# Performance work log

Hardware: AMD Instinct MI355X
Metric: run time of the kernel (lower is better)

Reference implementation:

```python
import jax, jax.numpy as jnp
import numpy as np

T, B, I, H, NH = 256, 8, 1024, 1024, 16
DH = H // NH
LN_EPS = 1e-5


def setup_inputs() -> dict:
    key = jax.random.key(0)
    ks = jax.random.split(key, 8)
    def w(k, shape, fan_in):
        return jax.random.normal(k, shape, jnp.float32) / np.float32(np.sqrt(fan_in))
    inputs = jax.random.normal(ks[0], (T, B, I), jnp.float32)
    # 4 HybridGates (forget, input, update, output) stacked: Linear(I+H -> H)
    W_gates = w(ks[1], (4, H, I + H), I + H)
    b_gates = jnp.zeros((4, H), jnp.float32)
    ln_g = jnp.ones((4, H), jnp.float32)   # LayerNorm weight per gate
    ln_b = jnp.zeros((4, H), jnp.float32)  # LayerNorm bias per gate
    # MultiheadAttention in_proj (split into q/k/v) and out_proj
    Wq = w(ks[2], (H, H), H); Wk = w(ks[3], (H, H), H); Wv = w(ks[4], (H, H), H)
    bq = jnp.zeros((H,), jnp.float32); bk = jnp.zeros((H,), jnp.float32); bv = jnp.zeros((H,), jnp.float32)
    Wo = w(ks[5], (H, H), H); bo = jnp.zeros((H,), jnp.float32)
    return dict(inputs=inputs, W_gates=W_gates, b_gates=b_gates, ln_g=ln_g, ln_b=ln_b,
                Wq=Wq, Wk=Wk, Wv=Wv, bq=bq, bk=bk, bv=bv, Wo=Wo, bo=bo)


def _layernorm(x, g, b):
    m = jnp.mean(x, axis=-1, keepdims=True)
    v = jnp.var(x, axis=-1, keepdims=True)
    return (x - m) * jax.lax.rsqrt(v + LN_EPS) * g + b


def reference(inputs, W_gates, b_gates, ln_g, ln_b, Wq, Wk, Wv, bq, bk, bv, Wo, bo):
    Tn, Bn, _ = inputs.shape
    scale = 1.0 / np.float32(np.sqrt(DH))
    pos = jnp.arange(Tn)

    def step(carry, x_t):
        hx, cx, Kb, Vb, t = carry  # Kb/Vb: [T, B, NH, DH] cached projections of past outputs
        combined = jnp.concatenate([x_t, hx], axis=1)          # [B, I+H]
        z = jnp.einsum('bd,khd->kbh', combined, W_gates) + b_gates[:, None, :]
        z = _layernorm(z, ln_g[:, None, :], ln_b[:, None, :])  # [4, B, H]
        f = jax.nn.sigmoid(z[0]); i = jax.nn.sigmoid(z[1])
        g = jnp.tanh(z[2]);       o = jax.nn.sigmoid(z[3])
        cx = f * cx + i * g
        h0 = o * jnp.tanh(cx)                                   # [B, H]
        # attention of current hidden over all previously produced outputs
        q = (h0 @ Wq.T + bq).reshape(Bn, NH, DH)
        scores = jnp.einsum('bhd,sbhd->bhs', q, Kb) * scale     # [B, NH, T]
        scores = jnp.where((pos < t)[None, None, :], scores, -1e9)
        attn = jax.nn.softmax(scores, axis=-1)
        ctx = jnp.einsum('bhs,sbhd->bhd', attn, Vb).reshape(Bn, H)
        attn_out = ctx @ Wo.T + bo
        hx = h0 + jnp.where(t > 0, attn_out, 0.0)               # no attention at t=0
        # cache k/v projections of the new output (linear, so per-token projection is exact)
        Kb = Kb.at[t].set((hx @ Wk.T + bk).reshape(Bn, NH, DH))
        Vb = Vb.at[t].set((hx @ Wv.T + bv).reshape(Bn, NH, DH))
        return (hx, cx, Kb, Vb, t + 1), hx

    init = (jnp.zeros((Bn, H), inputs.dtype), jnp.zeros((Bn, H), inputs.dtype),
            jnp.zeros((Tn, Bn, NH, DH), inputs.dtype), jnp.zeros((Tn, Bn, NH, DH), inputs.dtype),
            jnp.int32(0))
    (hx, cx, _, _, _), outputs = jax.lax.scan(step, init, inputs)
    return outputs, hx, cx
```

## Files before the change

kernel.cpp:

```cpp
#include <hip/hip_runtime.h>
#include <math.h>

#define NBLK 256
#define NTHR 512
#define GATHER 255

#define OFF_HX    0
#define OFF_H0    8192
#define OFF_CTX   16384
#define OFF_Z     24576
#define OFF_KB    57344
#define OFF_VB    (OFF_KB + 2097152)
#define OFF_FLAGS (OFF_VB + 2097152)
#define FLG_U32   (4096 + 128 + 2048)

#define S_WG    0
#define S_STAGE 32768
#define S_CX    36864
#define S_H0L   37888
#define S_Q     38912
#define S_PS    38976
#define S_RED   39232
#define S_R2    39248
#define S_EH    39264
#define S_ZX    39296
#define S_KVX   39424
#define LDS_FLOATS 39488
#define LDS_BYTES  (LDS_FLOATS * 4)

typedef unsigned long long u64;
union F2U { u64 u; float2 f; };

__device__ __forceinline__ float ld1(const float* p) {
    return __hip_atomic_load(const_cast<float*>(p), __ATOMIC_RELAXED, __HIP_MEMORY_SCOPE_AGENT);
}
__device__ __forceinline__ void st1(float* p, float v) {
    __hip_atomic_store(p, v, __ATOMIC_RELAXED, __HIP_MEMORY_SCOPE_AGENT);
}
__device__ __forceinline__ unsigned ldu(const unsigned* p) {
    return __hip_atomic_load(const_cast<unsigned*>(p), __ATOMIC_RELAXED, __HIP_MEMORY_SCOPE_AGENT);
}
__device__ __forceinline__ void stu(unsigned* p, unsigned v) {
    __hip_atomic_store(p, v, __ATOMIC_RELAXED, __HIP_MEMORY_SCOPE_AGENT);
}
__device__ __forceinline__ float2 ld2(const float* p) {
    F2U c; c.u = __hip_atomic_load(reinterpret_cast<u64*>(const_cast<float*>(p)),
                                   __ATOMIC_RELAXED, __HIP_MEMORY_SCOPE_AGENT);
    return c.f;
}
__device__ __forceinline__ void st2(float* p, float2 v) {
    F2U c; c.f = v;
    __hip_atomic_store(reinterpret_cast<u64*>(p), c.u,
                       __ATOMIC_RELAXED, __HIP_MEMORY_SCOPE_AGENT);
}
__device__ __forceinline__ float4 ld4(const float* p) {
    float2 a = ld2(p), b = ld2(p + 2);
    return make_float4(a.x, a.y, b.x, b.y);
}
__device__ __forceinline__ float dot4(const float4 a, const float4 b) {
    return a.x*b.x + a.y*b.y + a.z*b.z + a.w*b.w;
}

__device__ __forceinline__ void arrive(unsigned* flags, int blk, unsigned bc) {
    __syncthreads();
    if (threadIdx.x == 0) stu(flags + blk * 16, bc);
}
__device__ __forceinline__ void waitbar(unsigned* flags, unsigned* golines,
                                        unsigned bc, int blk) {
    if (blk == GATHER) {
        if (threadIdx.x < 256)
            while (ldu(flags + threadIdx.x * 16) < bc) __builtin_amdgcn_s_sleep(4);
        __syncthreads();
        if (threadIdx.x < 8) stu(golines + threadIdx.x * 16, bc);
    } else {
        if (threadIdx.x == 0)
            while (ldu(golines + (blk >> 5) * 16) < bc) __builtin_amdgcn_s_sleep(4);
    }
    __syncthreads();
}

__global__ __launch_bounds__(NTHR, 1)
void qlstm_kernel(const float* __restrict__ x,  const float* __restrict__ Wg,
                  const float* __restrict__ bg, const float* __restrict__ lng,
                  const float* __restrict__ lnb,const float* __restrict__ Wq,
                  const float* __restrict__ Wk, const float* __restrict__ Wv,
                  const float* __restrict__ bq, const float* __restrict__ bk,
                  const float* __restrict__ bv, const float* __restrict__ Wo,
                  const float* __restrict__ bo, float* __restrict__ out,
                  float* __restrict__ ws)
{
    extern __shared__ float lds[];
    const int blk = blockIdx.x, tid = threadIdx.x;
    const int w = tid >> 6, l = tid & 63;

    __builtin_amdgcn_fence(__ATOMIC_ACQUIRE, "agent");

    float* hx  = ws + OFF_HX;   float* h0g = ws + OFF_H0;
    float* ctx = ws + OFF_CTX;  float* z   = ws + OFF_Z;
    float* Kb  = ws + OFF_KB;   float* Vb  = ws + OFF_VB;
    unsigned* flags   = (unsigned*)(ws + OFF_FLAGS);
    unsigned* golines = flags + 4096;
    unsigned* cflg    = golines + 128;
    unsigned bc = 1;

    {
        const float* wsrc = Wg + (size_t)blk * 32768;
        #pragma unroll
        for (int j = 0; j < 16; ++j) {
            const int fi = j * 512 + tid;
            *(float4*)(lds + S_WG + fi * 4) = *(const float4*)(wsrc + fi * 4);
        }
    }
    const int kv_mat = blk >> 7;
    const int kv_h   = (blk & 127) * 8 + w;
    const float* kv_wrow = (kv_mat ? Wv : Wk) + (size_t)kv_h * 1024;
    float4 wkv[4];
    #pragma unroll
    for (int i = 0; i < 4; ++i) wkv[i] = *(const float4*)(kv_wrow + i * 256 + l * 4);
    const float kv_bias = (kv_mat ? bv : bk)[kv_h];
    const int g     = blk >> 6;
    const int hbase = (blk & 63) * 16;
    const int h0r   = hbase + 2 * w;
    const float bg0 = bg[g * 1024 + h0r], bg1 = bg[g * 1024 + h0r + 1];
    float lnw0[4], lnw1[4], lnb0v[4], lnb1v[4];
    #pragma unroll
    for (int g2 = 0; g2 < 4; ++g2) {
        lnw0[g2] = lng[g2 * 1024 + tid];       lnb0v[g2] = lnb[g2 * 1024 + tid];
        lnw1[g2] = lng[g2 * 1024 + 512 + tid]; lnb1v[g2] = lnb[g2 * 1024 + 512 + tid];
    }
    const int rg = blk >> 2, bp = blk & 3;
    const int er0 = rg * 16 + 2 * w;
    const int eb0 = bp * 2, eb1 = eb0 + 1;
    const float bor0 = bo[er0], bor1 = bo[er0 + 1];
    const int ab = blk >> 4, anh = blk & 15;
    const bool h0_writer = (blk < 128) && ((blk & 15) == 0);
    const int qdh = tid >> 3, qks = tid & 7;
    const float q_bias = (blk < 128) ? bq[anh * 64 + qdh] : 0.f;

    { const int gi = blk * NTHR + tid; if (gi < 8192) st1(hx + gi, 0.f); }
    if (tid < 256) *(float4*)(lds + S_CX + tid * 4) = make_float4(0,0,0,0);
    arrive(flags, blk, bc);

    for (int t = 0; t < 256; ++t) {
        float a0[8], a1[8];
        {
            const float* xt = x + (size_t)t * 8192;
            #pragma unroll
            for (int b = 0; b < 8; ++b) { a0[b] = 0.f; a1[b] = 0.f; }
            #pragma unroll
            for (int i = 0; i < 4; ++i) {
                const int k = i * 256 + l * 4;
                const float4 w0 = *(const float4*)(lds + S_WG + (2*w)   * 2048 + k);
                const float4 w1 = *(const float4*)(lds + S_WG + (2*w+1) * 2048 + k);
                #pragma unroll
                for (int b = 0; b < 8; ++b) {
                    const float4 a = *(const float4*)(xt + b * 1024 + k);
                    a0[b] += dot4(w0, a); a1[b] += dot4(w1, a);
                }
            }
        }
        waitbar(flags, golines, bc, blk);

        {
            float akv[8];
            #pragma unroll
            for (int b = 0; b < 8; ++b) akv[b] = 0.f;
            float2 hreg[8];
            #pragma unroll
            for (int c = 0; c < 2; ++c)
                #pragma unroll
                for (int j = 0; j < 4; ++j) {
                    const int idx = j * 512 + tid;
                    const int b = idx >> 8, off2 = idx & 255;
                    hreg[c * 4 + j] = ld2(hx + b * 1024 + c * 512 + off2 * 2);
                }
            #pragma unroll
            for (int c = 0; c < 2; ++c) {
                if (c) __syncthreads();
                #pragma unroll
                for (int j = 0; j < 4; ++j)
                    *(float2*)(lds + S_STAGE + (j * 512 + tid) * 2) = hreg[c * 4 + j];
                __syncthreads();
                #pragma unroll
                for (int ii = 0; ii < 2; ++ii) {
                    const int k = ii * 256 + l * 4;
                    const float4 w0 = *(const float4*)(lds + S_WG + (2*w)   * 2048 + 1024 + c * 512 + k);
                    const float4 w1 = *(const float4*)(lds + S_WG + (2*w+1) * 2048 + 1024 + c * 512 + k);
                    const float4 wk = wkv[c * 2 + ii];
                    #pragma unroll
                    for (int b = 0; b < 8; ++b) {
                        const float4 a = *(const float4*)(lds + S_STAGE + b * 512 + k);
                        a0[b] += dot4(w0, a); a1[b] += dot4(w1, a); akv[b] += dot4(wk, a);
                    }
                }
            }
            #pragma unroll
            for (int o = 1; o < 64; o <<= 1)
                #pragma unroll
                for (int b = 0; b < 8; ++b) {
                    a0[b]  += __shfl_xor(a0[b], o);
                    a1[b]  += __shfl_xor(a1[b], o);
                    akv[b] += __shfl_xor(akv[b], o);
                }
            if (l == 0) {
                #pragma unroll
                for (int b = 0; b < 8; ++b) {
                    lds[S_ZX + (2*w)   * 8 + b] = a0[b] + bg0;
                    lds[S_ZX + (2*w+1) * 8 + b] = a1[b] + bg1;
                    lds[S_KVX + w * 8 + b]      = akv[b] + kv_bias;
                }
            }
            __syncthreads();
            if (tid < 128) {
                const int h = tid & 15, b2 = tid >> 4;
                st1(z + (size_t)(g * 8 + b2) * 1024 + hbase + h, lds[S_ZX + h * 8 + b2]);
            } else if (tid < 192 && t > 0) {
                const int j = tid - 128;
                const int b2 = j >> 3, hh = j & 7;
                float* dst = kv_mat ? Vb : Kb;
                st1(dst + ((size_t)(t - 1) * 8 + b2) * 1024 + (blk & 127) * 8 + hh,
                    lds[S_KVX + hh * 8 + b2]);
            }
        }
        ++bc; arrive(flags, blk, bc);
        waitbar(flags, golines, bc, blk);

        if (blk < 128) {
            {
                float2 zreg[4];
                #pragma unroll
                for (int j = 0; j < 4; ++j) {
                    const int idx = j * 512 + tid;
                    const int g2 = idx >> 9, off2 = idx & 511;
                    zreg[j] = ld2(z + ((size_t)g2 * 8 + ab) * 1024 + off2 * 2);
                }
                #pragma unroll
                for (int j = 0; j < 4; ++j)
                    *(float2*)(lds + S_STAGE + (j * 512 + tid) * 2) = zreg[j];
            }
            __syncthreads();
            const int gt = w >> 1, hf = w & 1;
            float s = 0.f, q2s = 0.f;
            #pragma unroll
            for (int j = 0; j < 8; ++j) {
                const float v = lds[S_STAGE + gt * 1024 + hf * 512 + j * 64 + l];
                s += v; q2s += v * v;
            }
            #pragma unroll
            for (int o = 1; o < 64; o <<= 1) { s += __shfl_xor(s, o); q2s += __shfl_xor(q2s, o); }
            if (l == 0) { lds[S_RED + w] = s; lds[S_R2 + w] = q2s; }
            __syncthreads();
            float mean[4], rstd[4];
            #pragma unroll
            for (int g2 = 0; g2 < 4; ++g2) {
                const float ss = lds[S_RED + 2*g2] + lds[S_RED + 2*g2 + 1];
                const float qq = lds[S_R2  + 2*g2] + lds[S_R2  + 2*g2 + 1];
                const float m = ss * (1.f / 1024.f);
                mean[g2] = m;
                rstd[g2] = rsqrtf(qq * (1.f / 1024.f) - m * m + 1e-5f);
            }
            {
                float zv[4];
                #pragma unroll
                for (int g2 = 0; g2 < 4; ++g2)
                    zv[g2] = (lds[S_STAGE + g2 * 1024 + tid] - mean[g2]) * rstd[g2] * lnw0[g2] + lnb0v[g2];
                const float f  = 1.f / (1.f + __expf(-zv[0]));
                const float ii = 1.f / (1.f + __expf(-zv[1]));
                const float gg = tanhf(zv[2]);
                const float oo = 1.f / (1.f + __expf(-zv[3]));
                const float c  = f * lds[S_CX + tid] + ii * gg;
                lds[S_CX + tid] = c;
                const float ho = oo * tanhf(c);
                lds[S_H0L + tid] = ho;
                if (h0_writer) st1(h0g + ab * 1024 + tid, ho);
            }
            {
                float zv[4];
                #pragma unroll
                for (int g2 = 0; g2 < 4; ++g2)
                    zv[g2] = (lds[S_STAGE + g2 * 1024 + 512 + tid] - mean[g2]) * rstd[g2] * lnw1[g2] + lnb1v[g2];
                const float f  = 1.f / (1.f + __expf(-zv[0]));
                const float ii = 1.f / (1.f + __expf(-zv[1]));
                const float gg = tanhf(zv[2]);
                const float oo = 1.f / (1.f + __expf(-zv[3]));
                const float c  = f * lds[S_CX + 512 + tid] + ii * gg;
                lds[S_CX + 512 + tid] = c;
                const float ho = oo * tanhf(c);
                lds[S_H0L + 512 + tid] = ho;
                if (h0_writer) st1(h0g + ab * 1024 + 512 + tid, ho);
            }
            __syncthreads();
            {
                const float* wrow = Wq + (size_t)(anh * 64 + qdh) * 1024;
                float qa = 0.f;
                #pragma unroll 8
                for (int j = 0; j < 32; ++j) {
                    const int k = j * 32 + qks * 4;
                    qa += dot4(*(const float4*)(wrow + k), *(const float4*)(lds + S_H0L + k));
                }
                qa += __shfl_xor(qa, 1); qa += __shfl_xor(qa, 2); qa += __shfl_xor(qa, 4);
                if (qks == 0) lds[S_Q + qdh] = (qa + q_bias) * 0.125f;
            }
            __syncthreads();
            if (t > 0) {
                float sc = -1e30f;
                if (tid < t) {
                    const float* kr = Kb + ((size_t)tid * 8 + ab) * 1024 + anh * 64;
                    float d = 0.f;
                    #pragma unroll
                    for (int j = 0; j < 16; ++j) {
                        const float4 k4 = *(const float4*)(kr + j * 4);
                        d += k4.x*lds[S_Q + j*4]   + k4.y*lds[S_Q + j*4+1]
                           + k4.z*lds[S_Q + j*4+2] + k4.w*lds[S_Q + j*4+3];
                    }
                    sc = d;
                }
                float mx = sc;
                #pragma unroll
                for (int o = 1; o < 64; o <<= 1) mx = fmaxf(mx, __shfl_xor(mx, o));
                if (l == 0) lds[S_RED + w] = mx;
                __syncthreads();
                mx = lds[S_RED];
                #pragma unroll
                for (int j = 1; j < 8; ++j) mx = fmaxf(mx, lds[S_RED + j]);
                const float p = (tid < t) ? __expf(sc - mx) : 0.f;
                if (tid < 256) lds[S_PS + tid] = p;
                float ps = p;
                #pragma unroll
                for (int o = 1; o < 64; o <<= 1) ps += __shfl_xor(ps, o);
                if (l == 0) lds[S_R2 + w] = ps;
                __syncthreads();
                float tot = lds[S_R2];
                #pragma unroll
                for (int j = 1; j < 8; ++j) tot += lds[S_R2 + j];
                const float inv = 1.f / tot;
                const int dh2 = tid & 31, ss2 = tid >> 5;
                const float* vbase = Vb + (size_t)ab * 1024 + anh * 64 + dh2 * 2;
                float cax0 = 0.f, cay0 = 0.f, cax1 = 0.f, cay1 = 0.f;
                int s2 = ss2;
                for (; s2 + 48 < t; s2 += 64) {
                    const float2 va = *(const float2*)(vbase + (size_t)(s2)      * 8192);
                    const float2 vb = *(const float2*)(vbase + (size_t)(s2 + 16) * 8192);
                    const float2 vc = *(const float2*)(vbase + (size_t)(s2 + 32) * 8192);
                    const float2 vd = *(const float2*)(vbase + (size_t)(s2 + 48) * 8192);
                    const float pa = lds[S_PS + s2],      pb = lds[S_PS + s2 + 16];
                    const float pc = lds[S_PS + s2 + 32], pd = lds[S_PS + s2 + 48];
                    cax0 += pa * va.x; cay0 += pa * va.y;
                    cax1 += pb * vb.x; cay1 += pb * vb.y;
                    cax0 += pc * vc.x; cay0 += pc * vc.y;
                    cax1 += pd * vd.x; cay1 += pd * vd.y;
                }
                for (; s2 < t; s2 += 16) {
                    const float pp = lds[S_PS + s2];
                    const float2 v2 = *(const float2*)(vbase + (size_t)s2 * 8192);
                    cax0 += pp * v2.x; cay0 += pp * v2.y;
                }
                *(float2*)(lds + S_STAGE + tid * 2) = make_float2(cax0 + cax1, cay0 + cay1);
                __syncthreads();
                if (tid < 64) {
                    float v = 0.f;
                    #pragma unroll
                    for (int j = 0; j < 16; ++j) v += lds[S_STAGE + j * 64 + tid];
                    st1(ctx + ab * 1024 + anh * 64 + tid, v * inv);
                }
            }
            __syncthreads();
            if (tid == 0) stu(cflg + blk * 16, (unsigned)(t + 1));
        }

        {
            if (tid < 32) {
                const int pb = (tid < 16) ? eb0 : eb1;
                const unsigned* f = cflg + (pb * 16 + (tid & 15)) * 16;
                while (ldu(f) < (unsigned)(t + 1)) __builtin_amdgcn_s_sleep(2);
            }
            __syncthreads();
        }

        {
            if (tid < 16) {
                const int bsel = tid >> 3, hp = tid & 7;
                *(float2*)(lds + S_EH + bsel * 16 + hp * 2) =
                    ld2(h0g + (size_t)(eb0 + bsel) * 1024 + rg * 16 + hp * 2);
            }
            float o00 = 0.f, o01 = 0.f, o10 = 0.f, o11 = 0.f;
            if (t > 0) {
                float4 c0r[4], c1r[4];
                #pragma unroll
                for (int i = 0; i < 4; ++i) {
                    const int k = i * 256 + l * 4;
                    c0r[i] = ld4(ctx + (size_t)eb0 * 1024 + k);
                    c1r[i] = ld4(ctx + (size_t)eb1 * 1024 + k);
                }
                #pragma unroll
                for (int i = 0; i < 4; ++i) {
                    const int k = i * 256 + l * 4;
                    const float4 w0 = *(const float4*)(Wo + (size_t)er0 * 1024 + k);
                    const float4 w1 = *(const float4*)(Wo + (size_t)(er0+1) * 1024 + k);
                    o00 += dot4(w0, c0r[i]); o01 += dot4(w0, c1r[i]);
                    o10 += dot4(w1, c0r[i]); o11 += dot4(w1, c1r[i]);
                }
                #pragma unroll
                for (int o = 1; o < 64; o <<= 1) {
                    o00 += __shfl_xor(o00, o); o01 += __shfl_xor(o01, o);
                    o10 += __shfl_xor(o10, o); o11 += __shfl_xor(o11, o);
                }
            }
            __syncthreads();
            if (l == 0) {
                const float h00 = lds[S_EH + 2*w],      h10 = lds[S_EH + 2*w + 1];
                const float h01 = lds[S_EH + 16 + 2*w], h11 = lds[S_EH + 16 + 2*w + 1];
                const float v00 = (t > 0) ? h00 + o00 + bor0 : h00;
                const float v10 = (t > 0) ? h10 + o10 + bor1 : h10;
                const float v01 = (t > 0) ? h01 + o01 + bor0 : h01;
                const float v11 = (t > 0) ? h11 + o11 + bor1 : h11;
                st2(hx + eb0 * 1024 + er0, make_float2(v00, v10));
                st2(hx + eb1 * 1024 + er0, make_float2(v01, v11));
                *(float2*)(out + (size_t)t * 8192 + eb0 * 1024 + er0) = make_float2(v00, v10);
                *(float2*)(out + (size_t)t * 8192 + eb1 * 1024 + er0) = make_float2(v01, v11);
            }
        }
        ++bc; arrive(flags, blk, bc);
    }
    waitbar(flags, golines, bc, blk);

    if (h0_writer) {
        out[2097152 + 8192 + ab * 1024 + tid]       = lds[S_CX + tid];
        out[2097152 + 8192 + ab * 1024 + 512 + tid] = lds[S_CX + 512 + tid];
    }
    if (blk >= 136 && blk < 144) {
        const int b = blk - 136;
        out[2097152 + b * 1024 + tid]       = ld1(hx + b * 1024 + tid);
        out[2097152 + b * 1024 + 512 + tid] = ld1(hx + b * 1024 + 512 + tid);
    }
}

extern "C" void kernel_launch(void* const* d_in, const int* in_sizes, int n_in,
                              void* d_out, int out_size, void* d_ws, size_t ws_size,
                              hipStream_t stream) {
    const float* x   = (const float*)d_in[0];
    const float* Wg  = (const float*)d_in[1];
    const float* bg  = (const float*)d_in[2];
    const float* lng = (const float*)d_in[3];
    const float* lnb = (const float*)d_in[4];
    const float* Wq  = (const float*)d_in[5];
    const float* Wk  = (const float*)d_in[6];
    const float* Wv  = (const float*)d_in[7];
    const float* bq  = (const float*)d_in[8];
    const float* bk  = (const float*)d_in[9];
    const float* bv  = (const float*)d_in[10];
    const float* Wo  = (const float*)d_in[11];
    const float* bo  = (const float*)d_in[12];
    float* out = (float*)d_out;
    float* ws  = (float*)d_ws;

    static int attr_set = 0;
    if (!attr_set) {
        hipFuncSetAttribute((const void*)qlstm_kernel,
                            hipFuncAttributeMaxDynamicSharedMemorySize, LDS_BYTES);
        attr_set = 1;
    }
    hipMemsetAsync((char*)d_ws + (size_t)OFF_FLAGS * 4, 0, (size_t)FLG_U32 * 4, stream);

    void* args[] = { &x, &Wg, &bg, &lng, &lnb, &Wq, &Wk, &Wv,
                     &bq, &bk, &bv, &Wo, &bo, &out, &ws };
    hipLaunchCooperativeKernel((void*)qlstm_kernel, dim3(NBLK), dim3(NTHR),
                               args, LDS_BYTES, stream);
}
```

Measured before the change: 9.736 ms.

## Replace gather-block grid barrier with packed byte flags polled by every block

Swaps the two-level grid barrier (a gather block collects per-block flags, then broadcasts go-lines) for byte-sized per-block era flags packed into one 256-byte region. Each block polls all flags directly with 64 lanes reading 32-bit words. The second barrier now applies only to the 128 attention blocks, and the ctx-ready wait also uses packed byte flags. This removes a barrier hop and cache-line traffic per step, at the cost of every block polling shared lines, which adds contention, and 8-bit wraparound comparisons.

```diff
diff --git a/kernel.cpp b/kernel.cpp
--- a/kernel.cpp
+++ b/kernel.cpp
@@ -3,7 +3,6 @@
 
 #define NBLK 256
 #define NTHR 512
-#define GATHER 255
 
 #define OFF_HX    0
 #define OFF_H0    8192
@@ -12,7 +11,7 @@
 #define OFF_KB    57344
 #define OFF_VB    (OFF_KB + 2097152)
 #define OFF_FLAGS (OFF_VB + 2097152)
-#define FLG_U32   (4096 + 128 + 2048)
+#define FLG_U32   (64 + 32)
 
 #define S_WG    0
 #define S_STAGE 32768
@@ -29,6 +28,7 @@
 #define LDS_BYTES  (LDS_FLOATS * 4)
 
 typedef unsigned long long u64;
+typedef unsigned char u8;
 union F2U { u64 u; float2 f; };
 
 __device__ __forceinline__ float ld1(const float* p) {
@@ -39,9 +39,6 @@
 }
 __device__ __forceinline__ unsigned ldu(const unsigned* p) {
     return __hip_atomic_load(const_cast<unsigned*>(p), __ATOMIC_RELAXED, __HIP_MEMORY_SCOPE_AGENT);
-}
-__device__ __forceinline__ void stu(unsigned* p, unsigned v) {
-    __hip_atomic_store(p, v, __ATOMIC_RELAXED, __HIP_MEMORY_SCOPE_AGENT);
 }
 __device__ __forceinline__ float2 ld2(const float* p) {
     F2U c; c.u = __hip_atomic_load(reinterpret_cast<u64*>(const_cast<float*>(p)),
@@ -61,20 +58,24 @@
     return a.x*b.x + a.y*b.y + a.z*b.z + a.w*b.w;
 }
 
-__device__ __forceinline__ void arrive(unsigned* flags, int blk, unsigned bc) {
+__device__ __forceinline__ void arrive(u8* bflg, int blk, unsigned era) {
     __syncthreads();
-    if (threadIdx.x == 0) stu(flags + blk * 16, bc);
-}
-__device__ __forceinline__ void waitbar(unsigned* flags, unsigned* golines,
-                                        unsigned bc, int blk) {
-    if (blk == GATHER) {
-        if (threadIdx.x < 256)
-            while (ldu(flags + threadIdx.x * 16) < bc) __builtin_amdgcn_s_sleep(4);
-        __syncthreads();
-        if (threadIdx.x < 8) stu(golines + threadIdx.x * 16, bc);
-    } else {
-        if (threadIdx.x == 0)
-            while (ldu(golines + (blk >> 5) * 16) < bc) __builtin_amdgcn_s_sleep(4);
+    if (threadIdx.x == 0)
+        __hip_atomic_store(bflg + blk, (u8)(era & 0xFFu),
+                           __ATOMIC_RELAXED, __HIP_MEMORY_SCOPE_AGENT);
+}
+__device__ __forceinline__ void wait_all(const unsigned* bflg32, unsigned era) {
+    const unsigned e8 = era & 0xFFu;
+    if (threadIdx.x < 64) {
+        while (true) {
+            const unsigned v = ldu(bflg32 + threadIdx.x);
+            bool ok = true;
+            #pragma unroll
+            for (int k = 0; k < 4; ++k)
+                ok &= ((signed char)((((v >> (8*k)) & 0xFFu) - e8) & 0xFFu) >= 0);
+            if (__all(ok)) break;
+            __builtin_amdgcn_s_sleep(2);
+        }
     }
     __syncthreads();
 }
@@ -98,9 +99,10 @@
     float* hx  = ws + OFF_HX;   float* h0g = ws + OFF_H0;
     float* ctx = ws + OFF_CTX;  float* z   = ws + OFF_Z;
     float* Kb  = ws + OFF_KB;   float* Vb  = ws + OFF_VB;
-    unsigned* flags   = (unsigned*)(ws + OFF_FLAGS);
-    unsigned* golines = flags + 4096;
-    unsigned* cflg    = golines + 128;
+    u8* bflg = (u8*)(ws + OFF_FLAGS);
+    const unsigned* bflg32 = (const unsigned*)(ws + OFF_FLAGS);
+    u8* cflg = (u8*)(ws + OFF_FLAGS + 64);
+    const unsigned* cflg32 = (const unsigned*)(ws + OFF_FLAGS + 64);
     unsigned bc = 1;
 
     {
@@ -139,7 +141,7 @@
 
     { const int gi = blk * NTHR + tid; if (gi < 8192) st1(hx + gi, 0.f); }
     if (tid < 256) *(float4*)(lds + S_CX + tid * 4) = make_float4(0,0,0,0);
-    arrive(flags, blk, bc);
+    arrive(bflg, blk, bc);
 
     for (int t = 0; t < 256; ++t) {
         float a0[8], a1[8];
@@ -159,7 +161,7 @@
                 }
             }
         }
-        waitbar(flags, golines, bc, blk);
+        wait_all(bflg32, bc);
 
         {
             float akv[8];
@@ -222,10 +224,10 @@
                     lds[S_KVX + hh * 8 + b2]);
             }
         }
-        ++bc; arrive(flags, blk, bc);
-        waitbar(flags, golines, bc, blk);
+        ++bc; arrive(bflg, blk, bc);
 
         if (blk < 128) {
+            wait_all(bflg32, bc);
             {
                 float2 zreg[4];
                 #pragma unroll
@@ -365,14 +367,26 @@
                 }
             }
             __syncthreads();
-            if (tid == 0) stu(cflg + blk * 16, (unsigned)(t + 1));
+            if (tid == 0)
+                __hip_atomic_store(cflg + blk, (u8)((t + 1) & 0xFFu),
+                                   __ATOMIC_RELAXED, __HIP_MEMORY_SCOPE_AGENT);
         }
 
         {
-            if (tid < 32) {
-                const int pb = (tid < 16) ? eb0 : eb1;
-                const unsigned* f = cflg + (pb * 16 + (tid & 15)) * 16;
-                while (ldu(f) < (unsigned)(t + 1)) __builtin_amdgcn_s_sleep(2);
+            const unsigned e8 = (unsigned)((t + 1) & 0xFF);
+            if (tid < 64) {
+                const int base = eb0 * 4;
+                while (true) {
+                    bool ok = true;
+                    if (tid < 8) {
+                        const unsigned v = ldu(cflg32 + base + tid);
+                        #pragma unroll
+                        for (int k2 = 0; k2 < 4; ++k2)
+                            ok &= ((signed char)((((v >> (8*k2)) & 0xFFu) - e8) & 0xFFu) >= 0);
+                    }
+                    if (__all(ok)) break;
+                    __builtin_amdgcn_s_sleep(1);
+                }
             }
             __syncthreads();
         }
@@ -420,9 +434,9 @@
                 *(float2*)(out + (size_t)t * 8192 + eb1 * 1024 + er0) = make_float2(v01, v11);
             }
         }
-        ++bc; arrive(flags, blk, bc);
-    }
-    waitbar(flags, golines, bc, blk);
+        ++bc; arrive(bflg, blk, bc);
+    }
+    wait_all(bflg32, bc);
 
     if (h0_writer) {
         out[2097152 + 8192 + ab * 1024 + tid]       = lds[S_CX + tid];
```

Result: slower. 12.02 ms (+23.5%).
